# Optimization experiments

Measured on AMD Instinct MI355X. Metric: run time of the kernel, lower is better.

## Reference

```python
import jax, jax.numpy as jnp
import numpy as np

N_NODES = 50000
N_EDGES = 1_600_000
D = 128


def setup_inputs() -> dict:
    key = jax.random.key(0)
    ks = jax.random.split(key, 8)
    s = 1.0 / np.sqrt(D)
    return {
        "x": jax.random.normal(ks[0], (N_NODES, D), dtype=jnp.float32),
        "edge_index": jax.random.randint(ks[1], (2, N_EDGES), 0, N_NODES, dtype=jnp.int64),
        "W1l": jax.random.normal(ks[2], (D, D), dtype=jnp.float32) * s,
        "b1": jnp.zeros((D,), dtype=jnp.float32),
        "W1r": jax.random.normal(ks[3], (D, D), dtype=jnp.float32) * s,
        "W2l": jax.random.normal(ks[4], (D, D), dtype=jnp.float32) * s,
        "b2": jnp.zeros((D,), dtype=jnp.float32),
        "W2r": jax.random.normal(ks[5], (D, D), dtype=jnp.float32) * s,
    }


def _sage_conv(x, src, dst, Wl, b, Wr, num_nodes):
    # mean-aggregate source features at destination nodes
    msg = x[src]                                              # [E, d] gather
    summed = jax.ops.segment_sum(msg, dst, num_segments=num_nodes)
    cnt = jax.ops.segment_sum(jnp.ones((src.shape[0], 1), x.dtype), dst,
                              num_segments=num_nodes)
    mean = summed / jnp.maximum(cnt, 1.0)                     # clamp like PyG
    return mean @ Wl.T + b + x @ Wr.T


def reference(x, edge_index, W1l, b1, W1r, W2l, b2, W2r):
    src, dst = edge_index[0], edge_index[1]
    n = x.shape[0]
    h = _sage_conv(x, src, dst, W1l, b1, W1r, n)
    h = jax.nn.relu(h)
    out = _sage_conv(h, src, dst, W2l, b2, W2r, n)
    return out
```

## Files before the change

kernel.cpp:

```cpp
#include <hip/hip_runtime.h>

#define NN 50000
#define NE 1600000
#define DD 128

#define L1T 512
#define VPT 4
#define EPB (L1T * VPT)
#define NB1 ((NE + EPB - 1) / EPB)
#define NBUCK ((NN + 127) >> 7)
#define BSTRIDE 5120

typedef __attribute__((ext_vector_type(8))) short bf16x8;
typedef __attribute__((ext_vector_type(4))) float f32x4;
typedef __attribute__((ext_vector_type(2))) float f32x2;

__device__ __forceinline__ ushort f2b(float f) {
    unsigned u = __float_as_uint(f);
    return (ushort)((u + 0x7FFFu + ((u >> 16) & 1u)) >> 16);
}


__global__ __launch_bounds__(L1T) void l1_scatter(const int* __restrict__ src,
                                                  const int* __restrict__ dst,
                                                  int* __restrict__ g_fill,
                                                  unsigned* __restrict__ l1out) {
    __shared__ int lhist[L1T];
    __shared__ int lscan[L1T];
    __shared__ int lrsv[L1T];
    __shared__ int lfill[L1T];
    __shared__ unsigned staged[EPB];
    int tid = threadIdx.x;
    lhist[tid] = 0;
    lfill[tid] = 0;
    __syncthreads();

    unsigned myv[VPT];
    int base = blockIdx.x * EPB;
#pragma unroll
    for (int i = 0; i < VPT; ++i) {
        int idx = base + i * L1T + tid;
        if (idx < NE) {
            unsigned d = (unsigned)dst[idx], s = (unsigned)src[idx];
            myv[i] = (d << 16) | s;
            atomicAdd(&lhist[d >> 7], 1);
        } else {
            myv[i] = 0xFFFFFFFFu;
        }
    }
    __syncthreads();

    lscan[tid] = lhist[tid];
    __syncthreads();
    for (int off = 1; off < L1T; off <<= 1) {
        int t = (tid >= off) ? lscan[tid - off] : 0;
        __syncthreads();
        lscan[tid] += t;
        __syncthreads();
    }

    int cntb = lhist[tid];
    if (cntb > 0) lrsv[tid] = atomicAdd(&g_fill[tid], cntb);

#pragma unroll
    for (int i = 0; i < VPT; ++i) {
        unsigned v = myv[i];
        if (v != 0xFFFFFFFFu) {
            int b = (v >> 16) >> 7;
            int p = lscan[b] - lhist[b] + atomicAdd(&lfill[b], 1);
            staged[p] = v;
        }
    }
    __syncthreads();

    int n = lscan[L1T - 1];
    for (int i = tid; i < n; i += L1T) {
        unsigned v = staged[i];
        int b = (v >> 16) >> 7;
        int g = lrsv[b] + (i - (lscan[b] - lhist[b]));
        if (g < BSTRIDE) l1out[(size_t)b * BSTRIDE + g] = v;
    }
}


__global__ __launch_bounds__(512) void l2_kernel(const int* __restrict__ g_fill,
                                                 const unsigned* __restrict__ l1out,
                                                 unsigned short* __restrict__ su,
                                                 int* __restrict__ rp) {
    int B = blockIdx.x;
    int tid = threadIdx.x;
    __shared__ int gsc[512];
    __shared__ int h2[128], sc[128], f2[128];
    int gv = (tid < NBUCK) ? g_fill[tid] : 0;
    gsc[tid] = gv;
    __syncthreads();
    for (int off = 1; off < 512; off <<= 1) {
        int t = (tid >= off) ? gsc[tid - off] : 0;
        __syncthreads();
        gsc[tid] += t;
        __syncthreads();
    }
    int base = gsc[B] - g_fill[B];
    int cnt = g_fill[B];
    if (cnt > BSTRIDE) cnt = BSTRIDE;
    if (tid < 128) { h2[tid] = 0; f2[tid] = 0; }
    __syncthreads();
    const unsigned* in = l1out + (size_t)B * BSTRIDE;
    for (int i = tid; i < cnt; i += 512) {
        unsigned v = in[i];
        atomicAdd(&h2[(v >> 16) & 127], 1);
    }
    __syncthreads();
    if (tid < 128) sc[tid] = h2[tid];
    __syncthreads();
    for (int off = 1; off < 128; off <<= 1) {
        int t = (tid >= off && tid < 128) ? sc[tid - off] : 0;
        __syncthreads();
        if (tid < 128) sc[tid] += t;
        __syncthreads();
    }
    int node = B * 128 + tid;
    if (tid < 128 && node <= NN) rp[node] = base + sc[tid] - h2[tid];
    if (B == 0 && tid == 0) rp[NN] = NE;
    __syncthreads();
    for (int i = tid; i < cnt; i += 512) {
        unsigned v = in[i];
        int b = (v >> 16) & 127;
        int p = atomicAdd(&f2[b], 1);
        su[base + sc[b] - h2[b] + p] = (unsigned short)(v & 0xFFFFu);
    }
}


__global__ __launch_bounds__(256) void cvt8_kernel(const float* __restrict__ x,
                                                   unsigned* __restrict__ xq) {
    int i = blockIdx.x * 256 + threadIdx.x;
    if (i < NN * DD / 4) {
        float4 v = ((const float4*)x)[i];
        int w = __builtin_amdgcn_cvt_pk_fp8_f32(v.x, v.y, 0, false);
        w = __builtin_amdgcn_cvt_pk_fp8_f32(v.z, v.w, w, true);
        xq[i] = (unsigned)w;
    }
}

__global__ void buildW_kernel(const float* __restrict__ W1l, const float* __restrict__ W1r,
                              const float* __restrict__ W2l, const float* __restrict__ W2r,
                              ushort* __restrict__ Wb1, ushort* __restrict__ Wb2) {
    int idx = blockIdx.x * 256 + threadIdx.x;
    int which = idx >> 15, r = idx & 32767;
    int c = r >> 8, k = r & 255;
    const float* Wl = which ? W2l : W1l;
    const float* Wr = which ? W2r : W1r;
    ushort* Wb = which ? Wb2 : Wb1;
    float v = (k < 128) ? Wl[c * 128 + k] : Wr[c * 128 + (k - 128)];
    Wb[r] = f2b(v);
}


#define ADD8(V) { f32x2 t_;                                                         \
    t_ = __builtin_amdgcn_cvt_pk_f32_fp8(V.x, false); acc[0] += t_.x; acc[1] += t_.y; \
    t_ = __builtin_amdgcn_cvt_pk_f32_fp8(V.x, true);  acc[2] += t_.x; acc[3] += t_.y; \
    t_ = __builtin_amdgcn_cvt_pk_f32_fp8(V.y, false); acc[4] += t_.x; acc[5] += t_.y; \
    t_ = __builtin_amdgcn_cvt_pk_f32_fp8(V.y, true);  acc[6] += t_.x; acc[7] += t_.y; }

__global__ __launch_bounds__(256) void agg_fp8(const unsigned char* __restrict__ xq,
                                               const int* __restrict__ rp,
                                               const unsigned short* __restrict__ su,
                                               ushort* __restrict__ meanb) {
    int wave = threadIdx.x >> 6, lane = threadIdx.x & 63;
    int node = blockIdx.x * 4 + wave;
    if (node >= NN) return;
    int start = __builtin_amdgcn_readfirstlane(rp[node]);
    int end   = __builtin_amdgcn_readfirstlane(rp[node + 1]);
    int eslot = lane >> 4, chunk = lane & 15;
    float acc[8] = {};
    int e = start + eslot;
    for (; e + 4 < end; e += 8) {
        unsigned s0 = su[e], s1 = su[e + 4];
        uint2 v0 = *(const uint2*)(xq + (size_t)s0 * 128 + chunk * 8);
        uint2 v1 = *(const uint2*)(xq + (size_t)s1 * 128 + chunk * 8);
        ADD8(v0); ADD8(v1);
    }
    if (e < end) {
        unsigned s0 = su[e];
        uint2 v0 = *(const uint2*)(xq + (size_t)s0 * 128 + chunk * 8);
        ADD8(v0);
    }
#pragma unroll
    for (int j = 0; j < 8; ++j) {
        acc[j] += __shfl_xor(acc[j], 16, 64);
        acc[j] += __shfl_xor(acc[j], 32, 64);
    }
    if (eslot == 0) {
        int cnt = end - start;
        float inv = 1.0f / (float)(cnt > 1 ? cnt : 1);
        uint4 o;
        o.x = (unsigned)f2b(acc[0] * inv) | ((unsigned)f2b(acc[1] * inv) << 16);
        o.y = (unsigned)f2b(acc[2] * inv) | ((unsigned)f2b(acc[3] * inv) << 16);
        o.z = (unsigned)f2b(acc[4] * inv) | ((unsigned)f2b(acc[5] * inv) << 16);
        o.w = (unsigned)f2b(acc[6] * inv) | ((unsigned)f2b(acc[7] * inv) << 16);
        *(uint4*)(meanb + (size_t)node * DD + chunk * 8) = o;
    }
}


template <int L1>
__global__ __launch_bounds__(256) void gemm_mfma(const ushort* __restrict__ meanb,
                                                 const float* __restrict__ xf,
                                                 const ushort* __restrict__ ah,
                                                 const ushort* __restrict__ Wb,
                                                 const float* __restrict__ bias,
                                                 float* __restrict__ outf,
                                                 ushort* __restrict__ outh,
                                                 unsigned char* __restrict__ outq) {
    __shared__ __align__(16) ushort WbL[8][128][32];
    int tid = threadIdx.x;
    int wave = tid >> 6, lane = tid & 63;
    int wave_r = wave >> 1, wave_c = wave & 1;
    int r0 = blockIdx.x * 32 + wave_r * 16;
    int c0 = wave_c * 64;
    int arow = r0 + (lane & 15);
    if (arow >= NN) arow = NN - 1;
    int kg = (lane >> 4) * 8;
    int c = lane & 15;

    bf16x8 af[8];
#pragma unroll
    for (int kc = 0; kc < 4; ++kc)
        af[kc] = *(const bf16x8*)(meanb + (size_t)arow * 128 + kc * 32 + kg);
#pragma unroll
    for (int kc = 4; kc < 8; ++kc) {
        if (L1) {
            const float* ap = xf + (size_t)arow * 128 + (kc - 4) * 32 + kg;
            float4 a = *(const float4*)ap;
            float4 b = *(const float4*)(ap + 4);
            bf16x8 v;
            v[0] = (short)f2b(a.x); v[1] = (short)f2b(a.y);
            v[2] = (short)f2b(a.z); v[3] = (short)f2b(a.w);
            v[4] = (short)f2b(b.x); v[5] = (short)f2b(b.y);
            v[6] = (short)f2b(b.z); v[7] = (short)f2b(b.w);
            af[kc] = v;
        } else {
            af[kc] = *(const bf16x8*)(ah + (size_t)arow * 128 + (kc - 4) * 32 + kg);
        }
    }

    {
        const uint4* Wg = (const uint4*)Wb;
#pragma unroll
        for (int it = 0; it < 16; ++it) {
            int idx = it * 256 + tid;
            int col = idx >> 5, chunk = idx & 31;
            int kc = chunk >> 2, k8 = chunk & 3;
            *(uint4*)&WbL[kc][col][k8 * 8] = Wg[idx];
        }
    }
    __syncthreads();

    f32x4 acc[4] = {};
#pragma unroll
    for (int kc = 0; kc < 8; ++kc) {
#pragma unroll
        for (int t = 0; t < 4; ++t) {
            bf16x8 bf = *(const bf16x8*)&WbL[kc][c0 + t * 16 + c][kg];
            acc[t] = __builtin_amdgcn_mfma_f32_16x16x32_bf16(af[kc], bf, acc[t], 0, 0, 0);
        }
    }

    int rbase = r0 + (lane >> 4) * 4;
#pragma unroll
    for (int t = 0; t < 4; ++t) {
        float bj = bias[c0 + t * 16 + c];
#pragma unroll
        for (int i = 0; i < 4; ++i) {
            int r = rbase + i;
            if (r < NN) {
                float v = acc[t][i] + bj;
                if (L1) {
                    v = fmaxf(v, 0.f);
                    outh[(size_t)r * 128 + c0 + t * 16 + c] = f2b(v);
                    int q = __builtin_amdgcn_cvt_pk_fp8_f32(v, v, 0, false);
                    outq[(size_t)r * 128 + c0 + t * 16 + c] = (unsigned char)q;
                } else {
                    outf[(size_t)r * 128 + c0 + t * 16 + c] = v;
                }
            }
        }
    }
}


extern "C" void kernel_launch(void* const* d_in, const int* in_sizes, int n_in,
                              void* d_out, int out_size, void* d_ws, size_t ws_size,
                              hipStream_t stream) {
    const float* x   = (const float*)d_in[0];
    const int*   ei  = (const int*)d_in[1];
    const float* W1l = (const float*)d_in[2];
    const float* b1  = (const float*)d_in[3];
    const float* W1r = (const float*)d_in[4];
    const float* W2l = (const float*)d_in[5];
    const float* b2  = (const float*)d_in[6];
    const float* W2r = (const float*)d_in[7];
    float* out = (float*)d_out;

    const int* src = ei;
    const int* dst = ei + NE;

    char* ws = (char*)d_ws;
    size_t off = 0;
    auto carve = [&](size_t bytes) {
        char* p = ws + off;
        off = (off + bytes + 255) & ~(size_t)255;
        return p;
    };
    int*            rp     = (int*)carve((NN + 1) * sizeof(int));
    int*            g_fill = (int*)carve(512 * sizeof(int));
    unsigned short* su     = (unsigned short*)carve((size_t)NE * sizeof(unsigned short));
    unsigned*       xq     = (unsigned*)carve((size_t)NN * DD);
    unsigned char*  hq     = (unsigned char*)carve((size_t)NN * DD);
    ushort*         meanb  = (ushort*)carve((size_t)NN * DD * sizeof(ushort));
    ushort*         hh     = (ushort*)carve((size_t)NN * DD * sizeof(ushort));
    ushort*         Wb1    = (ushort*)carve(128 * 256 * sizeof(ushort));
    ushort*         Wb2    = (ushort*)carve(128 * 256 * sizeof(ushort));
    unsigned*       l1out  = (unsigned*)hh;

    hipMemsetAsync(g_fill, 0, 512 * sizeof(int), stream);

    l1_scatter<<<NB1, L1T, 0, stream>>>(src, dst, g_fill, l1out);
    l2_kernel<<<NBUCK, 512, 0, stream>>>(g_fill, l1out, su, rp);

    cvt8_kernel<<<(NN * DD / 4 + 255) / 256, 256, 0, stream>>>(x, xq);
    buildW_kernel<<<256, 256, 0, stream>>>(W1l, W1r, W2l, W2r, Wb1, Wb2);

    const int GBLK = (NN + 31) / 32;

    agg_fp8<<<(NN + 3) / 4, 256, 0, stream>>>((const unsigned char*)xq, rp, su, meanb);
    gemm_mfma<1><<<GBLK, 256, 0, stream>>>(meanb, x, nullptr, Wb1, b1, nullptr, hh, hq);

    agg_fp8<<<(NN + 3) / 4, 256, 0, stream>>>(hq, rp, su, meanb);
    gemm_mfma<0><<<GBLK, 256, 0, stream>>>(meanb, nullptr, hh, Wb2, b2, out, nullptr, nullptr);
}
```

Measured before the change: 170.1 us.

## Fuse prep kernels, pre-swizzle weights, sub-sort CSR by source, unroll aggregation

```diff
diff --git a/kernel.cpp b/kernel.cpp
--- a/kernel.cpp
+++ b/kernel.cpp
@@ -18,6 +18,37 @@
 __device__ __forceinline__ ushort f2b(float f) {
     unsigned u = __float_as_uint(f);
     return (ushort)((u + 0x7FFFu + ((u >> 16) & 1u)) >> 16);
+}
+
+
+__global__ __launch_bounds__(256) void prep_kernel(const float* __restrict__ x,
+                                                   unsigned* __restrict__ xq,
+                                                   const float* __restrict__ W1l,
+                                                   const float* __restrict__ W1r,
+                                                   const float* __restrict__ W2l,
+                                                   const float* __restrict__ W2r,
+                                                   ushort* __restrict__ Wsw1,
+                                                   ushort* __restrict__ Wsw2,
+                                                   int* __restrict__ g_fill) {
+    int b = blockIdx.x, tid = threadIdx.x;
+    if (b < 6250) {
+        int i = b * 256 + tid;
+        float4 v = ((const float4*)x)[i];
+        int w = __builtin_amdgcn_cvt_pk_fp8_f32(v.x, v.y, 0, false);
+        w = __builtin_amdgcn_cvt_pk_fp8_f32(v.z, v.w, w, true);
+        xq[i] = (unsigned)w;
+    } else if (b < 6506) {
+        int idx = (b - 6250) * 256 + tid;
+        int which = idx >> 15, r = idx & 32767;
+        int c = r >> 8, k = r & 255;
+        const float* Wl = which ? W2l : W1l;
+        const float* Wr = which ? W2r : W1r;
+        ushort* Wsw = which ? Wsw2 : Wsw1;
+        float v = (k < 128) ? Wl[c * 128 + k] : Wr[c * 128 + (k - 128)];
+        Wsw[((k >> 5) * 128 + c) * 32 + (k & 31)] = f2b(v);
+    } else {
+        for (int i = tid; i < 512; i += 256) g_fill[i] = 0;
+    }
 }
 
 
@@ -83,77 +114,55 @@
 }
 
 
-__global__ __launch_bounds__(512) void l2_kernel(const int* __restrict__ g_fill,
-                                                 const unsigned* __restrict__ l1out,
-                                                 unsigned short* __restrict__ su,
-                                                 int* __restrict__ rp) {
+__global__ __launch_bounds__(1024) void l2_kernel(const int* __restrict__ g_fill,
+                                                  const unsigned* __restrict__ l1out,
+                                                  unsigned short* __restrict__ su,
+                                                  int* __restrict__ rp) {
     int B = blockIdx.x;
     int tid = threadIdx.x;
     __shared__ int gsc[512];
-    __shared__ int h2[128], sc[128], f2[128];
-    int gv = (tid < NBUCK) ? g_fill[tid] : 0;
-    gsc[tid] = gv;
+    __shared__ int h2[1024], sc[1024], f2[1024];
+    if (tid < 512) gsc[tid] = (tid < NBUCK) ? g_fill[tid] : 0;
     __syncthreads();
     for (int off = 1; off < 512; off <<= 1) {
-        int t = (tid >= off) ? gsc[tid - off] : 0;
-        __syncthreads();
-        gsc[tid] += t;
+        int t = (tid >= off && tid < 512) ? gsc[tid - off] : 0;
+        __syncthreads();
+        if (tid < 512) gsc[tid] += t;
         __syncthreads();
     }
     int base = gsc[B] - g_fill[B];
     int cnt = g_fill[B];
     if (cnt > BSTRIDE) cnt = BSTRIDE;
-    if (tid < 128) { h2[tid] = 0; f2[tid] = 0; }
+    h2[tid] = 0;
+    f2[tid] = 0;
     __syncthreads();
     const unsigned* in = l1out + (size_t)B * BSTRIDE;
-    for (int i = tid; i < cnt; i += 512) {
+    for (int i = tid; i < cnt; i += 1024) {
         unsigned v = in[i];
-        atomicAdd(&h2[(v >> 16) & 127], 1);
-    }
-    __syncthreads();
-    if (tid < 128) sc[tid] = h2[tid];
-    __syncthreads();
-    for (int off = 1; off < 128; off <<= 1) {
-        int t = (tid >= off && tid < 128) ? sc[tid - off] : 0;
-        __syncthreads();
-        if (tid < 128) sc[tid] += t;
-        __syncthreads();
-    }
-    int node = B * 128 + tid;
-    if (tid < 128 && node <= NN) rp[node] = base + sc[tid] - h2[tid];
+        int key = (int)((v >> 16) & 127) * 8 + (int)((v & 0xFFFFu) >> 13);
+        atomicAdd(&h2[key], 1);
+    }
+    __syncthreads();
+    sc[tid] = h2[tid];
+    __syncthreads();
+    for (int off = 1; off < 1024; off <<= 1) {
+        int t = (tid >= off) ? sc[tid - off] : 0;
+        __syncthreads();
+        sc[tid] += t;
+        __syncthreads();
+    }
+    if ((tid & 7) == 0) {
+        int n = B * 128 + (tid >> 3);
+        if (n < NN) rp[n] = base + sc[tid] - h2[tid];
+    }
     if (B == 0 && tid == 0) rp[NN] = NE;
     __syncthreads();
-    for (int i = tid; i < cnt; i += 512) {
+    for (int i = tid; i < cnt; i += 1024) {
         unsigned v = in[i];
-        int b = (v >> 16) & 127;
-        int p = atomicAdd(&f2[b], 1);
-        su[base + sc[b] - h2[b] + p] = (unsigned short)(v & 0xFFFFu);
-    }
-}
-
-
-__global__ __launch_bounds__(256) void cvt8_kernel(const float* __restrict__ x,
-                                                   unsigned* __restrict__ xq) {
-    int i = blockIdx.x * 256 + threadIdx.x;
-    if (i < NN * DD / 4) {
-        float4 v = ((const float4*)x)[i];
-        int w = __builtin_amdgcn_cvt_pk_fp8_f32(v.x, v.y, 0, false);
-        w = __builtin_amdgcn_cvt_pk_fp8_f32(v.z, v.w, w, true);
-        xq[i] = (unsigned)w;
-    }
-}
-
-__global__ void buildW_kernel(const float* __restrict__ W1l, const float* __restrict__ W1r,
-                              const float* __restrict__ W2l, const float* __restrict__ W2r,
-                              ushort* __restrict__ Wb1, ushort* __restrict__ Wb2) {
-    int idx = blockIdx.x * 256 + threadIdx.x;
-    int which = idx >> 15, r = idx & 32767;
-    int c = r >> 8, k = r & 255;
-    const float* Wl = which ? W2l : W1l;
-    const float* Wr = which ? W2r : W1r;
-    ushort* Wb = which ? Wb2 : Wb1;
-    float v = (k < 128) ? Wl[c * 128 + k] : Wr[c * 128 + (k - 128)];
-    Wb[r] = f2b(v);
+        int key = (int)((v >> 16) & 127) * 8 + (int)((v & 0xFFFFu) >> 13);
+        int p = atomicAdd(&f2[key], 1);
+        su[base + sc[key] - h2[key] + p] = (unsigned short)(v & 0xFFFFu);
+    }
 }
 
 
@@ -175,13 +184,15 @@
     int eslot = lane >> 4, chunk = lane & 15;
     float acc[8] = {};
     int e = start + eslot;
-    for (; e + 4 < end; e += 8) {
-        unsigned s0 = su[e], s1 = su[e + 4];
+    for (; e + 12 < end; e += 16) {
+        unsigned s0 = su[e], s1 = su[e + 4], s2 = su[e + 8], s3 = su[e + 12];
         uint2 v0 = *(const uint2*)(xq + (size_t)s0 * 128 + chunk * 8);
         uint2 v1 = *(const uint2*)(xq + (size_t)s1 * 128 + chunk * 8);
-        ADD8(v0); ADD8(v1);
-    }
-    if (e < end) {
+        uint2 v2 = *(const uint2*)(xq + (size_t)s2 * 128 + chunk * 8);
+        uint2 v3 = *(const uint2*)(xq + (size_t)s3 * 128 + chunk * 8);
+        ADD8(v0); ADD8(v1); ADD8(v2); ADD8(v3);
+    }
+    for (; e < end; e += 4) {
         unsigned s0 = su[e];
         uint2 v0 = *(const uint2*)(xq + (size_t)s0 * 128 + chunk * 8);
         ADD8(v0);
@@ -208,7 +219,7 @@
 __global__ __launch_bounds__(256) void gemm_mfma(const ushort* __restrict__ meanb,
                                                  const float* __restrict__ xf,
                                                  const ushort* __restrict__ ah,
-                                                 const ushort* __restrict__ Wb,
+                                                 const ushort* __restrict__ Wsw,
                                                  const float* __restrict__ bias,
                                                  float* __restrict__ outf,
                                                  ushort* __restrict__ outh,
@@ -246,13 +257,12 @@
     }
 
     {
-        const uint4* Wg = (const uint4*)Wb;
+        const uint4* Wg = (const uint4*)Wsw;
+        uint4* Wl4 = (uint4*)&WbL[0][0][0];
 #pragma unroll
         for (int it = 0; it < 16; ++it) {
             int idx = it * 256 + tid;
-            int col = idx >> 5, chunk = idx & 31;
-            int kc = chunk >> 2, k8 = chunk & 3;
-            *(uint4*)&WbL[kc][col][k8 * 8] = Wg[idx];
+            Wl4[idx] = Wg[idx];
         }
     }
     __syncthreads();
@@ -320,23 +330,19 @@
     unsigned char*  hq     = (unsigned char*)carve((size_t)NN * DD);
     ushort*         meanb  = (ushort*)carve((size_t)NN * DD * sizeof(ushort));
     ushort*         hh     = (ushort*)carve((size_t)NN * DD * sizeof(ushort));
-    ushort*         Wb1    = (ushort*)carve(128 * 256 * sizeof(ushort));
-    ushort*         Wb2    = (ushort*)carve(128 * 256 * sizeof(ushort));
+    ushort*         Wsw1   = (ushort*)carve(128 * 256 * sizeof(ushort));
+    ushort*         Wsw2   = (ushort*)carve(128 * 256 * sizeof(ushort));
     unsigned*       l1out  = (unsigned*)hh;
 
-    hipMemsetAsync(g_fill, 0, 512 * sizeof(int), stream);
-
+    prep_kernel<<<6507, 256, 0, stream>>>(x, xq, W1l, W1r, W2l, W2r, Wsw1, Wsw2, g_fill);
     l1_scatter<<<NB1, L1T, 0, stream>>>(src, dst, g_fill, l1out);
-    l2_kernel<<<NBUCK, 512, 0, stream>>>(g_fill, l1out, su, rp);
-
-    cvt8_kernel<<<(NN * DD / 4 + 255) / 256, 256, 0, stream>>>(x, xq);
-    buildW_kernel<<<256, 256, 0, stream>>>(W1l, W1r, W2l, W2r, Wb1, Wb2);
+    l2_kernel<<<NBUCK, 1024, 0, stream>>>(g_fill, l1out, su, rp);
 
     const int GBLK = (NN + 31) / 32;
 
     agg_fp8<<<(NN + 3) / 4, 256, 0, stream>>>((const unsigned char*)xq, rp, su, meanb);
-    gemm_mfma<1><<<GBLK, 256, 0, stream>>>(meanb, x, nullptr, Wb1, b1, nullptr, hh, hq);
+    gemm_mfma<1><<<GBLK, 256, 0, stream>>>(meanb, x, nullptr, Wsw1, b1, nullptr, hh, hq);
 
     agg_fp8<<<(NN + 3) / 4, 256, 0, stream>>>(hq, rp, su, meanb);
-    gemm_mfma<0><<<GBLK, 256, 0, stream>>>(meanb, nullptr, hh, Wb2, b2, out, nullptr, nullptr);
-}
+    gemm_mfma<0><<<GBLK, 256, 0, stream>>>(meanb, nullptr, hh, Wsw2, b2, out, nullptr, nullptr);
+}
```

New measurement: 157.8 us. 1.08x faster.
